# Performance work log

Measured on AMD Instinct MI355X. Metric: run time of the kernel, lower is better.

Reference implementation:

```python
import jax, jax.numpy as jnp
import numpy as np

DEPTH = 8
HID = 512
EXP = 4
EPS = 1e-5


def setup_inputs() -> dict:
    key = jax.random.key(0)
    ks = jax.random.split(key, 12)
    B = 131072
    x = jax.random.normal(ks[0], (B, HID), dtype=jnp.float32)
    # input projection (input_dim=HID -> hidden_dim=HID)
    W_in = jax.random.normal(ks[1], (HID, HID), dtype=jnp.float32) * (1.0 / HID)
    b_in = jnp.zeros((HID,), dtype=jnp.float32)
    # stacked per-block params [DEPTH, ...]
    ln_g = jnp.ones((DEPTH, HID), dtype=jnp.float32)
    ln_b = jnp.zeros((DEPTH, HID), dtype=jnp.float32)
    W1 = jax.random.normal(ks[2], (DEPTH, HID, EXP), dtype=jnp.float32) * (1.0 / EXP)
    b1 = jnp.zeros((DEPTH, EXP), dtype=jnp.float32)
    W2 = jax.random.normal(ks[3], (DEPTH, EXP, HID), dtype=jnp.float32) * (1.0 / HID)
    b2 = jnp.zeros((DEPTH, HID), dtype=jnp.float32)
    # head (hidden_dim -> output_dim=HID)
    W_head = jax.random.normal(ks[4], (HID, HID), dtype=jnp.float32) * (1.0 / HID)
    b_head = jnp.zeros((HID,), dtype=jnp.float32)
    return {"x": x, "W_in": W_in, "b_in": b_in, "ln_g": ln_g, "ln_b": ln_b,
            "W1": W1, "b1": b1, "W2": W2, "b2": b2,
            "W_head": W_head, "b_head": b_head}


def _layernorm(x, g, b):
    mu = jnp.mean(x, axis=-1, keepdims=True)
    var = jnp.mean(jnp.square(x - mu), axis=-1, keepdims=True)
    return (x - mu) * jax.lax.rsqrt(var + EPS) * g + b


def reference(x, W_in, b_in, ln_g, ln_b, W1, b1, W2, b2, W_head, b_head):
    # mlp_input: Linear + relu (dropout=0.0 -> identity)
    h = jax.nn.relu(x @ W_in + b_in)  # [B, HID]

    def block(h, p):
        g, bb, w1, bb1, w2, bb2 = p
        z = _layernorm(h, g, bb)
        z = jax.nn.relu(z @ w1 + bb1)  # [B, EXP]
        z = z @ w2 + bb2               # [B, HID]
        return h + z, None

    h, _ = jax.lax.scan(block, h, (ln_g, ln_b, W1, b1, W2, b2))
    return h @ W_head + b_head
```

## Files before the change

### kernel.cpp

```cpp
#include <hip/hip_runtime.h>
#include <cstdint>

typedef unsigned short u16;
typedef unsigned int   u32;
typedef float  f32x4  __attribute__((ext_vector_type(4)));
typedef short  short8 __attribute__((ext_vector_type(8)));

__device__ inline float bf2f(u16 b){ u32 u=((u32)b)<<16; float f; __builtin_memcpy(&f,&u,4); return f; }
__device__ inline u16 f2bf(float f){ u32 u; __builtin_memcpy(&u,&f,4); u32 r=u+0x7FFFu+((u>>16)&1u); return (u16)(r>>16); }
__device__ inline float ubits(u32 u){ float f; __builtin_memcpy(&f,&u,4); return f; }
__device__ inline u32 pk(float hi, float lo){ u32 a,b; __builtin_memcpy(&a,&hi,4); __builtin_memcpy(&b,&lo,4); return __builtin_amdgcn_perm(a,b,0x07060302u); }
__device__ inline u32 cvtpk(float lo, float hi){ u32 r; asm("v_cvt_pk_bf16_f32 %0, %1, %2" : "=v"(r) : "v"(lo), "v"(hi)); return r; }
__device__ inline void gload_lds16(const void* g, void* l){
  __builtin_amdgcn_global_load_lds((const __attribute__((address_space(1))) unsigned int*)g,
                                   (__attribute__((address_space(3))) unsigned int*)l, 16, 0, 0);
}

#define CBAR(K) do{ asm volatile("s_waitcnt vmcnt(" #K ") lgkmcnt(0)" ::: "memory"); \
  __builtin_amdgcn_s_barrier(); __builtin_amdgcn_sched_barrier(0); }while(0)

__global__ __launch_bounds__(256) void prep_k(
    const float* __restrict__ W_in, const float* __restrict__ W_head,
    const float* __restrict__ ln_g, const float* __restrict__ W1,
    const float* __restrict__ W2, const float* __restrict__ b2,
    u16* __restrict__ Wt_in3, u16* __restrict__ Wt_hd3,
    u16* __restrict__ gw1f, u16* __restrict__ updA)
{
  int idx = blockIdx.x * 256 + threadIdx.x;
  if (idx < 524288){
    int which = idx >> 18;
    int q = idx & 262143;
    int t = q >> 14, o = q & 16383;
    int line = o >> 6, w = o & 63, slot = w >> 3, i = w & 7;
    int c8 = slot ^ (line & 7);
    int n = 2 * line + (c8 >> 2);
    int g = c8 & 3;
    if (which == 0){
      int k = t * 32 + g * 8 + i;
      Wt_in3[q] = f2bf(W_in[k * 512 + n]);
    } else {
      int k = t * 32 + (i < 4 ? 4 * g + i : 12 + 4 * g + i);
      Wt_hd3[q] = f2bf(W_head[k * 512 + n]);
    }
  } else if (idx < 544768){
    int q = idx - 524288;
    int d = q / 2560, r = q % 2560;
    int c = r / 160, r2 = r % 160;
    int g = r2 / 40, r3 = r2 % 40;
    int col = r3 >> 3, i = r3 & 7;
    int k = 32 * c + (i < 4 ? 4 * g + i : 12 + 4 * g + i);
    u16 v;
    if (col == 4) v = 0x3F80u;
    else          v = f2bf(ln_g[d * 512 + k] * W1[(d * 512 + k) * 4 + col]);
    gw1f[q] = v;
  } else if (idx < 577536){
    int q = idx - 544768;
    int d = q >> 12, r = q & 4095;
    int t = r >> 7, r2 = r & 127;
    int m = r2 >> 3, sl = r2 & 7;
    int k = 16 * t + m;
    u16 v = 0;
    if (sl < 4)       v = f2bf(W2[(d * 4 + sl) * 512 + k]);
    else if (sl == 4) v = f2bf(b2[d * 512 + k]);
    updA[q] = v;
  }
}

__global__ __launch_bounds__(64) void uv_k(
    const float* __restrict__ ln_g, const float* __restrict__ ln_b,
    const float* __restrict__ W1, const float* __restrict__ b1,
    float* __restrict__ U, float* __restrict__ V)
{
  int d = blockIdx.x >> 2, e = blockIdx.x & 3;
  int lane = threadIdx.x;
  float u = 0.f, v = 0.f;
  for (int k = lane; k < 512; k += 64){
    float w = W1[(d * 512 + k) * 4 + e];
    u += bf2f(f2bf(ln_g[d * 512 + k] * w));
    v += ln_b[d * 512 + k] * w;
  }
  for (int m = 1; m < 64; m <<= 1){ u += __shfl_xor(u, m); v += __shfl_xor(v, m); }
  if (lane == 0){ U[d * 4 + e] = u; V[d * 4 + e] = v + b1[d * 4 + e]; }
}

__global__ __launch_bounds__(512, 2) void fused_k(
    const float* __restrict__ x, const u16* __restrict__ Wt_in3,
    const float* __restrict__ b_in, const u16* __restrict__ Wt_hd3,
    const float* __restrict__ b_head, const u16* __restrict__ gw1f,
    const u16* __restrict__ updA, const float* __restrict__ U,
    const float* __restrict__ V, float* __restrict__ out)
{
  __shared__ __align__(16) char LT[147728];
  constexpr int SSo = 65536, ZBo = 77824;
  constexpr int MIDB = 98304, HXo = 98304;
  constexpr int UVo = 147456, SZo = 147712;
  float* sSf = (float*)(LT + SSo);
  float* zbf = (float*)(LT + ZBo);
  float* sUV = (float*)(LT + UVo);
  u16*   sZ  = (u16*)(LT + SZo);

  const int tid  = threadIdx.x;
  const int wv   = tid >> 6;
  const int lane = tid & 63;
  const int m    = lane & 15;
  const int g    = lane >> 4;
  const int nq   = wv & 3;
  const int rh   = wv >> 2;
  const size_t rowbase = (size_t)blockIdx.x * 128 + rh * 64;

  if (tid < 32) sUV[tid] = U[tid];
  else if (tid < 64) sUV[tid] = V[tid - 32];
  if (tid >= 64 && tid < 72) sZ[tid - 64] = 0;

  auto stageA = [&](const u16* W, int t, char* dst){
    const char* src = (const char*)(W + t * 16384) + tid * 16;
    char* d2 = dst + tid * 16;
    #pragma unroll
    for (int j = 0; j < 4; ++j)
      gload_lds16(src + j * 8192, d2 + j * 8192);
  };
  auto stageM = [&](int d, int bf3){
    char* dsg = LT + MIDB + bf3 * 16384;
    if (tid < 320)
      gload_lds16((const char*)gw1f + d * 5120 + tid * 16, dsg + tid * 16);
    gload_lds16((const char*)updA + d * 8192 + tid * 16, dsg + 5120 + tid * 16);
  };

  auto mkfrag = [&](f32x4 a, f32x4 b)->short8{
    union{u32 u[4]; short8 s;} t;
    t.u[0]=cvtpk(a[0],a[1]); t.u[1]=cvtpk(a[2],a[3]);
    t.u[2]=cvtpk(b[0],b[1]); t.u[3]=cvtpk(b[2],b[3]);
    return t.s;
  };
  auto mkfragT = [&](f32x4 a, f32x4 b)->short8{
    union{u32 u[4]; short8 s;} t;
    t.u[0]=pk(a[1],a[0]); t.u[1]=pk(a[3],a[2]);
    t.u[2]=pk(b[1],b[0]); t.u[3]=pk(b[3],b[2]);
    return t.s;
  };

  const int afoff = (m >> 1) * 128 + (((((m & 1) << 2) | g) ^ ((m >> 1) & 7)) << 4);

  f32x4 hv[4][4][2];
  #pragma unroll
  for (int q = 0; q < 4; ++q)
    #pragma unroll
    for (int c2 = 0; c2 < 4; ++c2){ hv[q][c2][0] = (f32x4)0.f; hv[q][c2][1] = (f32x4)0.f; }

  const float* xbase = x + (rowbase + m) * 512 + g * 8;
  f32x4 xA[4][2], xB[4][2];
  #pragma unroll
  for (int q = 0; q < 4; ++q){
    xA[q][0] = *(const f32x4*)(xbase + q * 8192);
    xA[q][1] = *(const f32x4*)(xbase + q * 8192 + 4);
    xB[q][0] = *(const f32x4*)(xbase + q * 8192 + 32);
    xB[q][1] = *(const f32x4*)(xbase + q * 8192 + 36);
  }
  stageA(Wt_in3, 0, LT);
  stageA(Wt_in3, 1, LT + 32768);
  __syncthreads();

  #pragma unroll
  for (int t = 0; t < 16; ++t){
    if (t < 14) stageA(Wt_in3, t + 2, LT + ((t + 2) % 3) * 32768);
    short8 bq[4];
    #pragma unroll
    for (int q = 0; q < 4; ++q)
      bq[q] = (t & 1) ? mkfrag(xB[q][0], xB[q][1]) : mkfrag(xA[q][0], xA[q][1]);
    if (t < 14){
      #pragma unroll
      for (int q = 0; q < 4; ++q){
        if (t & 1){
          xB[q][0] = *(const f32x4*)(xbase + q * 8192 + (t + 2) * 32);
          xB[q][1] = *(const f32x4*)(xbase + q * 8192 + (t + 2) * 32 + 4);
        } else {
          xA[q][0] = *(const f32x4*)(xbase + q * 8192 + (t + 2) * 32);
          xA[q][1] = *(const f32x4*)(xbase + q * 8192 + (t + 2) * 32 + 4);
        }
      }
    }
    const char* wb = LT + (t % 3) * 32768 + nq * 8192 + afoff;
    #pragma unroll
    for (int f = 0; f < 8; ++f){
      short8 aw = *(const short8*)(wb + f * 1024);
      #pragma unroll
      for (int q = 0; q < 4; ++q)
        hv[q][f >> 1][f & 1] =
          __builtin_amdgcn_mfma_f32_16x16x32_bf16(aw, bq[q], hv[q][f >> 1][f & 1], 0, 0, 0);
    }
    if (t < 14)       CBAR(20);
    else if (t == 14) CBAR(8);
  }

  #pragma unroll
  for (int q = 0; q < 4; ++q)
    #pragma unroll
    for (int c2 = 0; c2 < 4; ++c2)
      #pragma unroll
      for (int hf = 0; hf < 2; ++hf){
        f32x4 bi = *(const f32x4*)(b_in + nq * 128 + c2 * 32 + hf * 16 + g * 4);
        f32x4 v;
        #pragma unroll
        for (int r = 0; r < 4; ++r){ float w = hv[q][c2][hf][r] + bi[r]; v[r] = w > 0.f ? w : 0.f; }
        u32 ua = cvtpk(v[0], v[1]), ub = cvtpk(v[2], v[3]);
        hv[q][c2][hf][0] = ubits(ua << 16);
        hv[q][c2][hf][1] = ubits(ua & 0xFFFF0000u);
        hv[q][c2][hf][2] = ubits(ub << 16);
        hv[q][c2][hf][3] = ubits(ub & 0xFFFF0000u);
      }

  stageM(0, 0);
  stageM(1, 1);
  __syncthreads();

  #pragma unroll 1
  for (int d = 0; d < 8; ++d){
    if (d < 6)       stageM(d + 2, (d + 2) % 3);
    else if (d == 6) stageA(Wt_hd3, 0, LT);
    else             stageA(Wt_hd3, 1, LT + 32768);

    const u16* sGp = (const u16*)(LT + MIDB + (d % 3) * 16384);
    const u16* sAp = sGp + 2560;

    const u16* gb = (m < 5) ? (sGp + nq * 640 + g * 40 + m * 8) : sZ;
    const int gstep = (m < 5) ? 160 : 0;
    f32x4 aS[4], aG[4];
    #pragma unroll
    for (int q = 0; q < 4; ++q){ aS[q] = (f32x4)0.f; aG[q] = (f32x4)0.f; }
    #pragma unroll
    for (int c2 = 0; c2 < 4; ++c2){
      short8 bf = *(const short8*)(gb + c2 * gstep);
      #pragma unroll
      for (int q = 0; q < 4; ++q){
        short8 af = mkfragT(hv[q][c2][0], hv[q][c2][1]);
        aS[q] = __builtin_amdgcn_mfma_f32_16x16x32_bf16(af, bf, aS[q], 0, 0, 0);
        aG[q] = __builtin_amdgcn_mfma_f32_16x16x32_bf16(af, af, aG[q], 0, 0, 0);
      }
    }

    #pragma unroll
    for (int q = 0; q < 4; ++q){
      if (m < 5)
        *(f32x4*)(sSf + (((rh * 4 + q) * 4 + nq) * 6 + m) * 16 + 4 * g) = aS[q];
      if ((m >> 2) == g)
        sSf[(((rh * 4 + q) * 4 + nq) * 6 + 5) * 16 + m] = aG[q][m & 3];
    }
    CBAR(8);

    if (tid < 128){
      int rh2 = tid >> 6, rl = tid & 63, q2 = rl >> 4, b = rl & 15;
      float S0 = 0.f, S1 = 0.f, S2 = 0.f, S3 = 0.f, sm = 0.f, sq = 0.f;
      #pragma unroll
      for (int nn = 0; nn < 4; ++nn){
        const float* pp = sSf + (((rh2 * 4 + q2) * 4 + nn) * 6) * 16 + b;
        S0 += pp[0]; S1 += pp[16]; S2 += pp[32]; S3 += pp[48];
        sm += pp[64]; sq += pp[80];
      }
      float mu  = sm * (1.f / 512.f);
      float var = sq * (1.f / 512.f) - mu * mu;
      float rs  = rsqrtf(var + 1e-5f);
      f32x4 zz;
      float z0 = fmaf(rs, S0 - mu * sUV[d * 4 + 0], sUV[32 + d * 4 + 0]);
      float z1 = fmaf(rs, S1 - mu * sUV[d * 4 + 1], sUV[32 + d * 4 + 1]);
      float z2 = fmaf(rs, S2 - mu * sUV[d * 4 + 2], sUV[32 + d * 4 + 2]);
      float z3 = fmaf(rs, S3 - mu * sUV[d * 4 + 3], sUV[32 + d * 4 + 3]);
      zz[0] = z0 > 0.f ? z0 : 0.f;
      zz[1] = z1 > 0.f ? z1 : 0.f;
      zz[2] = z2 > 0.f ? z2 : 0.f;
      zz[3] = z3 > 0.f ? z3 : 0.f;
      *(f32x4*)(zbf + tid * 4) = zz;
    }
    CBAR(8);

    #pragma unroll
    for (int q = 0; q < 4; ++q){
      f32x4 z4 = *(const f32x4*)(zbf + (rh * 64 + q * 16 + m) * 4);
      union{u32 u[4]; short8 s;} bz;
      bz.u[0] = (g == 0) ? pk(z4[1], z4[0]) : 0u;
      bz.u[1] = (g == 0) ? pk(z4[3], z4[2]) : 0u;
      bz.u[2] = (g == 0) ? 0x00003F80u : 0u;
      bz.u[3] = 0u;
      const u16* ab = (g == 0) ? (sAp + nq * 1024 + m * 8) : sZ;
      const int ainc = (g == 0) ? 128 : 0;
      #pragma unroll
      for (int t2 = 0; t2 < 8; ++t2){
        short8 aw = *(const short8*)(ab + t2 * ainc);
        hv[q][t2 >> 1][t2 & 1] =
          __builtin_amdgcn_mfma_f32_16x16x32_bf16(aw, bz.s, hv[q][t2 >> 1][t2 & 1], 0, 0, 0);
      }
    }
    CBAR(1);
  }

  short8 p[4][4];
  #pragma unroll
  for (int q = 0; q < 4; ++q)
    #pragma unroll
    for (int c2 = 0; c2 < 4; ++c2)
      p[q][c2] = mkfrag(hv[q][c2][0], hv[q][c2][1]);

  f32x4 acc[4][8];
  #pragma unroll
  for (int q = 0; q < 4; ++q)
    #pragma unroll
    for (int of = 0; of < 8; ++of) acc[q][of] = (f32x4)0.f;

  if (nq == 0){
    #pragma unroll
    for (int q = 0; q < 4; ++q)
      *(short8*)(LT + HXo + rh * 4096 + (q * 64 + m * 4 + g) * 16) = p[q][0];
  }
  CBAR(8);

  #pragma unroll
  for (int c = 0; c < 16; ++c){
    if (c < 14) stageA(Wt_hd3, c + 2, LT + ((c + 2) % 3) * 32768);
    if (c < 15 && nq == ((c + 1) >> 2)){
      #pragma unroll
      for (int q = 0; q < 4; ++q)
        *(short8*)(LT + HXo + ((c + 1) & 1) * 8192 + rh * 4096 + (q * 64 + m * 4 + g) * 16)
          = p[q][(c + 1) & 3];
    }
    const char* hxb = LT + HXo + (c & 1) * 8192 + rh * 4096 + (m * 4 + g) * 16;
    short8 bh[4];
    #pragma unroll
    for (int q = 0; q < 4; ++q) bh[q] = *(const short8*)(hxb + q * 1024);
    const char* wb = LT + (c % 3) * 32768 + nq * 8192 + afoff;
    #pragma unroll
    for (int of = 0; of < 8; ++of){
      short8 aw = *(const short8*)(wb + of * 1024);
      #pragma unroll
      for (int q = 0; q < 4; ++q)
        acc[q][of] = __builtin_amdgcn_mfma_f32_16x16x32_bf16(aw, bh[q], acc[q][of], 0, 0, 0);
    }
    if (c < 14)       CBAR(4);
    else if (c == 14) CBAR(0);
  }

  #pragma unroll
  for (int q = 0; q < 4; ++q)
    #pragma unroll
    for (int of = 0; of < 8; ++of){
      f32x4 bhd = *(const f32x4*)(b_head + nq * 128 + of * 16 + g * 4);
      f32x4 v;
      #pragma unroll
      for (int r = 0; r < 4; ++r) v[r] = acc[q][of][r] + bhd[r];
      *(f32x4*)(out + (rowbase + q * 16 + m) * 512 + nq * 128 + of * 16 + g * 4) = v;
    }
}

extern "C" void kernel_launch(void* const* d_in, const int* in_sizes, int n_in,
                              void* d_out, int out_size, void* d_ws, size_t ws_size,
                              hipStream_t stream)
{
  const float* x      = (const float*)d_in[0];
  const float* W_in   = (const float*)d_in[1];
  const float* b_in   = (const float*)d_in[2];
  const float* ln_g   = (const float*)d_in[3];
  const float* ln_b   = (const float*)d_in[4];
  const float* W1     = (const float*)d_in[5];
  const float* b1     = (const float*)d_in[6];
  const float* W2     = (const float*)d_in[7];
  const float* b2     = (const float*)d_in[8];
  const float* W_head = (const float*)d_in[9];
  const float* b_head = (const float*)d_in[10];
  float* out = (float*)d_out;
  const int B = in_sizes[0] / 512;

  char* ws = (char*)d_ws;
  u16*   Wt_in3 = (u16*)ws;
  u16*   Wt_hd3 = Wt_in3 + 262144;
  u16*   gw1f   = Wt_hd3 + 262144;
  u16*   updA   = gw1f + 20480;
  float* Up     = (float*)(updA + 32768);
  float* Vp     = Up + 32;

  prep_k<<<2256, 256, 0, stream>>>(W_in, W_head, ln_g, W1, W2, b2, Wt_in3, Wt_hd3, gw1f, updA);
  uv_k<<<32, 64, 0, stream>>>(ln_g, ln_b, W1, b1, Up, Vp);
  fused_k<<<B / 128, 512, 0, stream>>>(x, Wt_in3, b_in, Wt_hd3, b_head, gw1f, updA, Up, Vp, out);
}
```

Before: 338.2 us.

## Rework LDS weight staging into four slots with paired K-chunks per barrier

Reorganizes the LDS layout so the weight staging area uses four 32KB slots instead of three. The input GEMM now processes two K-chunks per iteration with one barrier, halving the number of barriers. The mid-block loop moves prefetch issue after the reduction barrier, drops its trailing barrier, and uses full vmcnt(0) waits. The head GEMM uses a four-slot ring. The aim is to cut barrier and synchronization overhead and improve overlap, at the risk of more live registers and LDS slot reuse hazards from the changed barrier placement.

```diff
diff --git a/kernel.cpp b/kernel.cpp
--- a/kernel.cpp
+++ b/kernel.cpp
@@ -91,8 +91,9 @@
     const float* __restrict__ V, float* __restrict__ out)
 {
   __shared__ __align__(16) char LT[147728];
-  constexpr int SSo = 65536, ZBo = 77824;
-  constexpr int MIDB = 98304, HXo = 98304;
+  constexpr int MIDB = 0;
+  constexpr int SSo = 49152, ZBo = 61440;
+  constexpr int HXo = 131072;
   constexpr int UVo = 147456, SZo = 147712;
   float* sSf = (float*)(LT + SSo);
   float* zbf = (float*)(LT + ZBo);
@@ -112,9 +113,9 @@
   else if (tid < 64) sUV[tid] = V[tid - 32];
   if (tid >= 64 && tid < 72) sZ[tid - 64] = 0;
 
-  auto stageA = [&](const u16* W, int t, char* dst){
-    const char* src = (const char*)(W + t * 16384) + tid * 16;
-    char* d2 = dst + tid * 16;
+  auto stage4 = [&](const u16* W, int T, int slot){
+    const char* src = (const char*)(W + T * 16384) + tid * 16;
+    char* d2 = LT + slot * 32768 + tid * 16;
     #pragma unroll
     for (int j = 0; j < 4; ++j)
       gload_lds16(src + j * 8192, d2 + j * 8192);
@@ -148,48 +149,53 @@
     for (int c2 = 0; c2 < 4; ++c2){ hv[q][c2][0] = (f32x4)0.f; hv[q][c2][1] = (f32x4)0.f; }
 
   const float* xbase = x + (rowbase + m) * 512 + g * 8;
-  f32x4 xA[4][2], xB[4][2];
-  #pragma unroll
-  for (int q = 0; q < 4; ++q){
-    xA[q][0] = *(const f32x4*)(xbase + q * 8192);
-    xA[q][1] = *(const f32x4*)(xbase + q * 8192 + 4);
-    xB[q][0] = *(const f32x4*)(xbase + q * 8192 + 32);
-    xB[q][1] = *(const f32x4*)(xbase + q * 8192 + 36);
-  }
-  stageA(Wt_in3, 0, LT);
-  stageA(Wt_in3, 1, LT + 32768);
-  __syncthreads();
-
-  #pragma unroll
-  for (int t = 0; t < 16; ++t){
-    if (t < 14) stageA(Wt_in3, t + 2, LT + ((t + 2) % 3) * 32768);
-    short8 bq[4];
-    #pragma unroll
-    for (int q = 0; q < 4; ++q)
-      bq[q] = (t & 1) ? mkfrag(xB[q][0], xB[q][1]) : mkfrag(xA[q][0], xA[q][1]);
-    if (t < 14){
-      #pragma unroll
-      for (int q = 0; q < 4; ++q){
-        if (t & 1){
-          xB[q][0] = *(const f32x4*)(xbase + q * 8192 + (t + 2) * 32);
-          xB[q][1] = *(const f32x4*)(xbase + q * 8192 + (t + 2) * 32 + 4);
-        } else {
-          xA[q][0] = *(const f32x4*)(xbase + q * 8192 + (t + 2) * 32);
-          xA[q][1] = *(const f32x4*)(xbase + q * 8192 + (t + 2) * 32 + 4);
+  f32x4 xr[4][2][2];
+  #pragma unroll
+  for (int q = 0; q < 4; ++q)
+    #pragma unroll
+    for (int ch = 0; ch < 2; ++ch){
+      xr[q][ch][0] = *(const f32x4*)(xbase + q * 8192 + ch * 32);
+      xr[q][ch][1] = *(const f32x4*)(xbase + q * 8192 + ch * 32 + 4);
+    }
+  stage4(Wt_in3, 0, 0);
+  stage4(Wt_in3, 1, 1);
+  CBAR(0);
+
+  #pragma unroll
+  for (int t = 0; t < 8; ++t){
+    if (t < 7){
+      stage4(Wt_in3, 2 * t + 2, (2 * t + 2) & 3);
+      stage4(Wt_in3, 2 * t + 3, (2 * t + 3) & 3);
+      __builtin_amdgcn_sched_barrier(0);
+    }
+    short8 bq[2][4];
+    #pragma unroll
+    for (int ch = 0; ch < 2; ++ch)
+      #pragma unroll
+      for (int q = 0; q < 4; ++q)
+        bq[ch][q] = mkfrag(xr[q][ch][0], xr[q][ch][1]);
+    if (t < 7){
+      #pragma unroll
+      for (int q = 0; q < 4; ++q)
+        #pragma unroll
+        for (int ch = 0; ch < 2; ++ch){
+          xr[q][ch][0] = *(const f32x4*)(xbase + q * 8192 + (t + 1) * 64 + ch * 32);
+          xr[q][ch][1] = *(const f32x4*)(xbase + q * 8192 + (t + 1) * 64 + ch * 32 + 4);
         }
-      }
-    }
-    const char* wb = LT + (t % 3) * 32768 + nq * 8192 + afoff;
-    #pragma unroll
-    for (int f = 0; f < 8; ++f){
-      short8 aw = *(const short8*)(wb + f * 1024);
-      #pragma unroll
-      for (int q = 0; q < 4; ++q)
-        hv[q][f >> 1][f & 1] =
-          __builtin_amdgcn_mfma_f32_16x16x32_bf16(aw, bq[q], hv[q][f >> 1][f & 1], 0, 0, 0);
-    }
-    if (t < 14)       CBAR(20);
-    else if (t == 14) CBAR(8);
+    }
+    #pragma unroll
+    for (int ch = 0; ch < 2; ++ch){
+      const char* wb = LT + ((2 * t + ch) & 3) * 32768 + nq * 8192 + afoff;
+      #pragma unroll
+      for (int f = 0; f < 8; ++f){
+        short8 aw = *(const short8*)(wb + f * 1024);
+        #pragma unroll
+        for (int q = 0; q < 4; ++q)
+          hv[q][f >> 1][f & 1] =
+            __builtin_amdgcn_mfma_f32_16x16x32_bf16(aw, bq[ch][q], hv[q][f >> 1][f & 1], 0, 0, 0);
+      }
+    }
+    if (t < 7) CBAR(16);
   }
 
   #pragma unroll
@@ -209,16 +215,13 @@
         hv[q][c2][hf][3] = ubits(ub & 0xFFFF0000u);
       }
 
+  __syncthreads();
   stageM(0, 0);
   stageM(1, 1);
-  __syncthreads();
+  CBAR(0);
 
   #pragma unroll 1
   for (int d = 0; d < 8; ++d){
-    if (d < 6)       stageM(d + 2, (d + 2) % 3);
-    else if (d == 6) stageA(Wt_hd3, 0, LT);
-    else             stageA(Wt_hd3, 1, LT + 32768);
-
     const u16* sGp = (const u16*)(LT + MIDB + (d % 3) * 16384);
     const u16* sAp = sGp + 2560;
 
@@ -245,7 +248,11 @@
       if ((m >> 2) == g)
         sSf[(((rh * 4 + q) * 4 + nq) * 6 + 5) * 16 + m] = aG[q][m & 3];
     }
-    CBAR(8);
+    CBAR(0);
+
+    if (d < 6)       stageM(d + 2, (d + 2) % 3);
+    else if (d == 6) stage4(Wt_hd3, 0, 2);
+    else             stage4(Wt_hd3, 1, 3);
 
     if (tid < 128){
       int rh2 = tid >> 6, rl = tid & 63, q2 = rl >> 4, b = rl & 15;
@@ -289,7 +296,6 @@
           __builtin_amdgcn_mfma_f32_16x16x32_bf16(aw, bz.s, hv[q][t2 >> 1][t2 & 1], 0, 0, 0);
       }
     }
-    CBAR(1);
   }
 
   short8 p[4][4];
@@ -310,11 +316,14 @@
     for (int q = 0; q < 4; ++q)
       *(short8*)(LT + HXo + rh * 4096 + (q * 64 + m * 4 + g) * 16) = p[q][0];
   }
-  CBAR(8);
+  CBAR(0);
 
   #pragma unroll
   for (int c = 0; c < 16; ++c){
-    if (c < 14) stageA(Wt_hd3, c + 2, LT + ((c + 2) % 3) * 32768);
+    if (c < 14){
+      stage4(Wt_hd3, c + 2, c & 3);
+      __builtin_amdgcn_sched_barrier(0);
+    }
     if (c < 15 && nq == ((c + 1) >> 2)){
       #pragma unroll
       for (int q = 0; q < 4; ++q)
@@ -325,7 +334,7 @@
     short8 bh[4];
     #pragma unroll
     for (int q = 0; q < 4; ++q) bh[q] = *(const short8*)(hxb + q * 1024);
-    const char* wb = LT + (c % 3) * 32768 + nq * 8192 + afoff;
+    const char* wb = LT + ((c + 2) & 3) * 32768 + nq * 8192 + afoff;
     #pragma unroll
     for (int of = 0; of < 8; ++of){
       short8 aw = *(const short8*)(wb + of * 1024);
```

Result: no change. 342.1 us (+1.1%).
